# Performance work log

Hardware: AMD Instinct MI355X
Metric: run time of the kernel (lower is better)

Reference implementation:

```python
import jax, jax.numpy as jnp
import numpy as np
import math

B, S, D, H, WIN = 2, 4096, 512, 8, 50
DK = D // H


def setup_inputs() -> dict:
    key = jax.random.key(0)
    ks = jax.random.split(key, 10)
    scale = 0.02
    return {
        "x": jax.random.normal(ks[0], (B, S, D), dtype=jnp.float32),
        "opcode_types": jax.random.randint(ks[1], (B, S), 0, 10, dtype=jnp.int64),
        "Wq": jax.random.normal(ks[2], (D, D), dtype=jnp.float32) * scale,
        "bq": jnp.zeros((D,), dtype=jnp.float32),
        "Wk": jax.random.normal(ks[3], (D, D), dtype=jnp.float32) * scale,
        "bk": jnp.zeros((D,), dtype=jnp.float32),
        "Wv": jax.random.normal(ks[4], (D, D), dtype=jnp.float32) * scale,
        "bv": jnp.zeros((D,), dtype=jnp.float32),
        "Wo": jax.random.normal(ks[5], (D, D), dtype=jnp.float32) * scale,
        "bo": jnp.zeros((D,), dtype=jnp.float32),
    }


def reference(x, opcode_types, Wq, bq, Wk, bk, Wv, bv, Wo, bo):
    b, s, d = x.shape
    # Linear projections (torch Linear: x @ W.T + b), split heads -> [B,H,S,DK]
    q = (x @ Wq.T + bq).reshape(b, s, H, DK).transpose(0, 2, 1, 3)
    k = (x @ Wk.T + bk).reshape(b, s, H, DK).transpose(0, 2, 1, 3)
    v = (x @ Wv.T + bv).reshape(b, s, H, DK).transpose(0, 2, 1, 3)

    pos = jnp.arange(s)
    window = jnp.abs(pos[:, None] - pos[None, :]) <= WIN          # [S,S]
    ctrl_cols = (opcode_types == 0).any(axis=0)                   # [S]
    allow = window | ctrl_cols[None, :]                           # [S,S]

    scores = jnp.einsum("bhqd,bhkd->bhqk", q, k) / math.sqrt(DK)  # [B,H,S,S]
    scores = jnp.where(allow[None, None], scores, jnp.float32(-1e9))
    attn = jax.nn.softmax(scores, axis=-1)
    attn = jnp.nan_to_num(attn, nan=0.0)
    out = jnp.einsum("bhqk,bhkd->bhqd", attn, v)                  # [B,H,S,DK]
    out = out.transpose(0, 2, 1, 3).reshape(b, s, d)
    return out @ Wo.T + bo
```

## Files before the change

kernel.cpp:

```cpp
#include <hip/hip_runtime.h>
#include <hip/hip_bf16.h>
#include <math.h>

#define B_ 2
#define S_ 4096
#define D_ 512
#define H_ 8
#define DK_ 64
#define WIN_ 50
#define NGT 32
#define QSCALE 0.18033688011112042f

typedef __attribute__((ext_vector_type(8))) _Float16 half8;
typedef __attribute__((ext_vector_type(4))) float f32x4;
typedef __attribute__((ext_vector_type(4))) unsigned short us4;
typedef unsigned short ushort_t;

__device__ __forceinline__ unsigned short f2h(float f) {
    _Float16 h = (_Float16)f;
    return __builtin_bit_cast(unsigned short, h);
}
__device__ __forceinline__ unsigned cvt_pk_f16(float lo, float hi) {
    unsigned r;
    asm("v_cvt_pkrtz_f16_f32 %0, %1, %2" : "=v"(r) : "v"(lo), "v"(hi));
    return r;
}
__device__ __forceinline__ float v_exp2(float x) {
    float r;
    asm("v_exp_f32 %0, %1\n\ts_nop 0" : "=v"(r) : "v"(x));
    return r;
}

__global__ __launch_bounds__(256) void prep_all(const float* __restrict__ x,
                                                const float* __restrict__ W0,
                                                const float* __restrict__ W1,
                                                const float* __restrict__ W2,
                                                const float* __restrict__ W3,
                                                const int* __restrict__ opcode,
                                                ushort_t* __restrict__ xh,
                                                ushort_t* __restrict__ whb,
                                                int* __restrict__ glist,
                                                int* __restrict__ gcount) {
    const int bid = blockIdx.x;
    const int t = threadIdx.x;
    if (bid < 4096) {
        int i = bid * 256 + t;
        f32x4 v = ((const f32x4*)x)[i];
        us4 hv;
        for (int e = 0; e < 4; ++e) hv[e] = f2h(v[e]);
        ((us4*)xh)[i] = hv;
    } else if (bid < 5120) {
        int b2 = bid - 4096;
        int wz = b2 >> 8, inner = b2 & 255;
        const float* src = (wz == 0) ? W0 : (wz == 1) ? W1 : (wz == 2) ? W2 : W3;
        int i = inner * 256 + t;
        f32x4 v = ((const f32x4*)src)[i];
        us4 hv;
        for (int e = 0; e < 4; ++e) hv[e] = f2h(v[e]);
        ((us4*)(whb + (size_t)wz * D_ * D_))[i] = hv;
    } else {
        __shared__ int cnts[256];
        unsigned fl = 0; int c = 0;
        for (int k = 0; k < 16; ++k) {
            int col = t * 16 + k;
            int flag = (opcode[col] == 0) | (opcode[S_ + col] == 0);
            fl |= (unsigned)flag << k; c += flag;
        }
        cnts[t] = c;
        __syncthreads();
        for (int off = 1; off < 256; off <<= 1) {
            int v = cnts[t];
            int a = (t >= off) ? cnts[t - off] : 0;
            __syncthreads();
            cnts[t] = v + a;
            __syncthreads();
        }
        int base = cnts[t] - c;
        for (int k = 0; k < 16; ++k)
            if ((fl >> k) & 1) glist[base++] = t * 16 + k;
        int G = cnts[255];
        if (t == 255) gcount[0] = G;
        for (int k = 0; k < 8; ++k) {
            int idx = G + t + k * 256;
            if (idx < S_) glist[idx] = -1;
        }
    }
}

__device__ __forceinline__ void gemm_core1(const ushort_t* __restrict__ A,
                                           const ushort_t* __restrict__ Bw,
                                           ushort_t (&LDS)[2][8192],
                                           int m0, int n0, int t,
                                           f32x4 (&acc)[4][4]) {
    const int lane = t & 63, wave = t >> 6;
    const int lrow = lane & 15, lkg = lane >> 4;
    const int wr = wave >> 1, wc = wave & 1;
    const ushort_t* srcs[2] = {A, Bw};
    const int row0[2] = {m0, n0};

    auto stage = [&](int buf, int k0) {
        #pragma unroll
        for (int it = 0; it < 4; ++it) {
            int c = it * 4 + wave;
            int tile = c >> 3;
            int kg = (c >> 1) & 3;
            int r = ((c & 1) << 6) | lane;
            const ushort_t* g = srcs[tile] + (size_t)(row0[tile] + r) * 512 + k0 + kg * 8;
            __builtin_amdgcn_global_load_lds(
                (const __attribute__((address_space(1))) void*)g,
                (__attribute__((address_space(3))) void*)(&LDS[buf][c * 512]),
                16, 0, 0);
        }
    };

    stage(0, 0);
    __syncthreads();

    const int aoff = lkg * 1024 + (wr * 64 + lrow) * 8;
    const int boff = 4096 + lkg * 1024 + (wc * 64 + lrow) * 8;
    int cur = 0;
    for (int ks = 0; ks < 16; ++ks) {
        if (ks < 15) stage(cur ^ 1, (ks + 1) * 32);
        const ushort_t* Lb = LDS[cur];
        half8 ah[4], bh[4];
        #pragma unroll
        for (int m = 0; m < 4; ++m) ah[m] = *(const half8*)(Lb + aoff + m * 128);
        #pragma unroll
        for (int n = 0; n < 4; ++n) bh[n] = *(const half8*)(Lb + boff + n * 128);
        #pragma unroll
        for (int m = 0; m < 4; ++m)
            #pragma unroll
            for (int n = 0; n < 4; ++n)
                acc[m][n] = __builtin_amdgcn_mfma_f32_16x16x32_f16(ah[m], bh[n], acc[m][n], 0, 0, 0);
        __syncthreads();
        cur ^= 1;
    }
}

__global__ __launch_bounds__(256) void gemm_qkv(const ushort_t* __restrict__ xh,
                                                const ushort_t* __restrict__ whb,
                                                const float* __restrict__ bq,
                                                const float* __restrict__ bk,
                                                const float* __restrict__ bv,
                                                ushort_t* __restrict__ qb,
                                                char* __restrict__ bandimg) {
    __shared__ ushort_t LDS[2][8192];
    const int z = blockIdx.z;
    const int t = threadIdx.x;
    const ushort_t* Wz = whb + (size_t)z * D_ * D_;
    const int lane = t & 63, wave = t >> 6;
    const int lrow = lane & 15, lkg = lane >> 4;
    const int wr = wave >> 1, wc = wave & 1;

    f32x4 acc[4][4];
    for (int m = 0; m < 4; ++m)
        for (int n = 0; n < 4; ++n)
            acc[m][n] = f32x4{0.f, 0.f, 0.f, 0.f};

    if (z == 2) {
        const int m0 = blockIdx.y * 128, n0 = blockIdx.x * 128;
        gemm_core1(xh, Wz, LDS, m0, n0, t, acc);
        for (int m = 0; m < 4; ++m) {
            int s_base = m0 + wr * 64 + m * 16 + lkg * 4;
            int bb = s_base >> 12, s0 = s_base & (S_ - 1);
            int jt = s0 >> 6, jr0 = s0 & 63;
            for (int n = 0; n < 4; ++n) {
                int col = n0 + wc * 64 + n * 16 + lrow;
                float bs = bv[col];
                int hh = col >> 6, dk = col & 63;
                us4 pk;
                for (int r = 0; r < 4; ++r) pk[r] = f2h(acc[m][n][r] + bs);
                char* img = bandimg + (((size_t)(bb * H_ + hh)) * 64 + jt) * 16384 + 8192;
                *(us4*)(img + ((dk * 128 + jr0 * 2) ^ ((dk & 7) << 4))) = pk;
            }
        }
    } else {
        const int m0 = blockIdx.x * 128, n0 = blockIdx.y * 128;
        gemm_core1(Wz, xh, LDS, m0, n0, t, acc);
        const float* bias = (z == 0) ? bq : bk;
        for (int m = 0; m < 4; ++m) {
            int d_base = m0 + wr * 64 + m * 16 + lkg * 4;
            f32x4 b4 = *(const f32x4*)(bias + d_base);
            int hh = d_base >> 6, dkb = d_base & 63;
            for (int n = 0; n < 4; ++n) {
                int s = n0 + wc * 64 + n * 16 + lrow;
                int bb = s >> 12, sl = s & (S_ - 1);
                us4 pk;
                if (z == 0) {
                    for (int r = 0; r < 4; ++r) pk[r] = f2h((acc[m][n][r] + b4[r]) * QSCALE);
                    *(us4*)(qb + (((size_t)(bb * H_ + hh) * S_) + sl) * DK_ + dkb) = pk;
                } else {
                    for (int r = 0; r < 4; ++r) pk[r] = f2h(acc[m][n][r] + b4[r]);
                    int jt = sl >> 6, jr = sl & 63;
                    char* img = bandimg + (((size_t)(bb * H_ + hh)) * 64 + jt) * 16384;
                    *(us4*)(img + ((jr * 128 + dkb * 2) ^ ((jr & 7) << 4))) = pk;
                }
            }
        }
    }
}

__global__ __launch_bounds__(256) void gemm_fin(const ushort_t* __restrict__ Woh,
                                                const ushort_t* __restrict__ aoh,
                                                const float* __restrict__ bias,
                                                float* __restrict__ outp) {
    __shared__ ushort_t LDS[2][6144];
    const int t = threadIdx.x;
    const int lane = t & 63, wave = t >> 6;
    const int lrow = lane & 15, lkg = lane >> 4;
    const int wr = wave >> 1, wc = wave & 1;
    const int m0 = blockIdx.x * 64, n0 = blockIdx.y * 128;

    auto stage = [&](int buf, int k0) {
        #pragma unroll
        for (int it = 0; it < 3; ++it) {
            int c = it * 4 + wave;
            const ushort_t* g;
            if (c < 4) {
                g = Woh + (size_t)(m0 + lane) * 512 + k0 + c * 8;
            } else {
                int s2 = c - 4;
                int kg = s2 >> 1, rh = s2 & 1;
                g = aoh + (size_t)(n0 + rh * 64 + lane) * 512 + k0 + kg * 8;
            }
            __builtin_amdgcn_global_load_lds(
                (const __attribute__((address_space(1))) void*)g,
                (__attribute__((address_space(3))) void*)(&LDS[buf][c * 512]),
                16, 0, 0);
        }
    };

    f32x4 acc[2][4];
    for (int m = 0; m < 2; ++m)
        for (int n = 0; n < 4; ++n)
            acc[m][n] = f32x4{0.f, 0.f, 0.f, 0.f};

    stage(0, 0);
    __syncthreads();

    const int aoff = lkg * 512 + (wr * 32 + lrow) * 8;
    const int boff = 2048 + lkg * 1024 + (wc * 64 + lrow) * 8;
    int cur = 0;
    for (int ks = 0; ks < 16; ++ks) {
        if (ks < 15) stage(cur ^ 1, (ks + 1) * 32);
        const ushort_t* Lb = LDS[cur];
        half8 ah[2], bh[4];
        #pragma unroll
        for (int m = 0; m < 2; ++m) ah[m] = *(const half8*)(Lb + aoff + m * 128);
        #pragma unroll
        for (int n = 0; n < 4; ++n) bh[n] = *(const half8*)(Lb + boff + n * 128);
        #pragma unroll
        for (int m = 0; m < 2; ++m)
            #pragma unroll
            for (int n = 0; n < 4; ++n)
                acc[m][n] = __builtin_amdgcn_mfma_f32_16x16x32_f16(ah[m], bh[n], acc[m][n], 0, 0, 0);
        __syncthreads();
        cur ^= 1;
    }

    for (int m = 0; m < 2; ++m) {
        int d_base = m0 + wr * 32 + m * 16 + lkg * 4;
        f32x4 b4 = *(const f32x4*)(bias + d_base);
        for (int n = 0; n < 4; ++n) {
            int s = n0 + wc * 64 + n * 16 + lrow;
            f32x4 o;
            for (int r = 0; r < 4; ++r) o[r] = acc[m][n][r] + b4[r];
            *(f32x4*)(outp + (size_t)s * D_ + d_base) = o;
        }
    }
}

__global__ __launch_bounds__(256) void prep_glob(const char* __restrict__ bandimg,
                                                 char* __restrict__ globimg,
                                                 const int* __restrict__ glist,
                                                 const int* __restrict__ gcount) {
    int G = gcount[0];
    int gc = blockIdx.x;
    if (gc * 64 >= G) return;
    int h = blockIdx.y, b = blockIdx.z;
    int t = threadIdx.x;
    __shared__ int jl[64];
    if (t < 64) { int gi = gc * 64 + t; jl[t] = (gi < G) ? glist[gi] : -1; }
    __syncthreads();
    const size_t bh = (size_t)(b * H_ + h);
    char* dst = globimg + (bh * NGT + gc) * 16384;
    {
        int c = t >> 2, q = t & 3;
        int jj = jl[c];
        #pragma unroll
        for (int p = 0; p < 2; ++p) {
            int o_dst = c * 128 + q * 32 + p * 16;
            __attribute__((ext_vector_type(8))) short val;
            if (jj >= 0) {
                int jr = jj & 63, jt = jj >> 6;
                const char* src = bandimg + (bh * 64 + jt) * 16384;
                val = *(const __attribute__((ext_vector_type(8))) short*)
                      (src + ((jr * 128 + q * 32 + p * 16) ^ ((jr & 7) << 4)));
            } else {
                for (int e = 0; e < 8; ++e) val[e] = 0;
            }
            *(__attribute__((ext_vector_type(8))) short*)(dst + (o_dst ^ ((c & 7) << 4))) = val;
        }
    }
    {
        int d = t >> 2, qq = t & 3;
        __attribute__((ext_vector_type(8))) short v0, v1;
        #pragma unroll 16
        for (int i = 0; i < 16; ++i) {
            int c = qq * 16 + i;
            int jj = jl[c];
            ushort_t val = 0;
            if (jj >= 0) {
                int jr = jj & 63, jt = jj >> 6;
                const char* src = bandimg + (bh * 64 + jt) * 16384 + 8192;
                val = *(const ushort_t*)(src + ((d * 128 + jr * 2) ^ ((d & 7) << 4)));
            }
            if (i < 8) v0[i] = val; else v1[i - 8] = val;
        }
        int o = d * 128 + qq * 32;
        *(__attribute__((ext_vector_type(8))) short*)(dst + 8192 + (o ^ ((d & 7) << 4))) = v0;
        *(__attribute__((ext_vector_type(8))) short*)(dst + 8192 + ((o + 16) ^ ((d & 7) << 4))) = v1;
    }
}

__global__ __launch_bounds__(512) void attn_mfma6(const ushort_t* __restrict__ Qp,
                                                  const char* __restrict__ bandimg,
                                                  const char* __restrict__ globimg,
                                                  const int* __restrict__ glist,
                                                  const int* __restrict__ gcount,
                                                  ushort_t* __restrict__ AO) {
    __shared__ char buf[2][16384];
    __shared__ ushort_t Ps[8 * 16 * 64];

    const int t = threadIdx.x, lane = t & 63, wave = t >> 6;
    const int q = lane & 15, g = lane >> 4;
    const int bid = blockIdx.x;
    const int bh_lin = bid & 15;
    const int b = bh_lin >> 3, h = bh_lin & 7;
    const int i0 = (bid >> 4) * 128;
    const size_t headoff = ((size_t)(b * H_ + h)) * S_ * DK_;
    const int iq = i0 + wave * 16 + q;
    const int iqm = iq - WIN_;

    half8 qa[2];
    {
        const ushort_t* qrow = Qp + headoff + (size_t)iq * DK_;
        qa[0] = *(const half8*)(qrow + 8 * g);
        qa[1] = *(const half8*)(qrow + 32 + 8 * g);
    }

    f32x4 Oa[4];
    for (int n = 0; n < 4; ++n) Oa[n] = f32x4{0.f, 0.f, 0.f, 0.f};
    float m_st = -1e30f, l_st = 0.f;

    int jlo = i0 - WIN_;
    int jt_lo = (jlo < 0) ? 0 : (jlo >> 6);
    int jhi = i0 + 127 + WIN_; if (jhi > S_ - 1) jhi = S_ - 1;
    int jt_hi = jhi >> 6;
    int nband = jt_hi - jt_lo + 1;
    const int G = gcount[0];
    int nglob = (G + 63) >> 6; if (nglob > NGT) nglob = NGT;
    int nchunk = nband + nglob;

    const size_t bh = (size_t)(b * H_ + h);

    unsigned needmask = 0;
    {
        int wmin = i0 - WIN_, wmax = i0 + 127 + WIN_;
        for (int gc = 0; gc < nglob; ++gc) {
            int lo = glist[gc * 64];
            int hidx = (gc * 64 + 63 < G) ? (gc * 64 + 63) : (G - 1);
            int hi = glist[hidx];
            bool nm = (lo <= wmax && hi >= wmin) || (gc == nglob - 1 && (G & 63));
            needmask |= (unsigned)nm << gc;
        }
    }

    int koff[4][2], poffw[4], poffr[2];
    #pragma unroll
    for (int n = 0; n < 4; ++n) {
        int row = n * 16 + q;
        #pragma unroll
        for (int kt = 0; kt < 2; ++kt)
            koff[n][kt] = (row * 128 + g * 16 + kt * 64) ^ ((row & 7) << 4);
        poffw[n] = (q * 128 + n * 32 + g * 8) ^ ((q & 7) << 4);
    }
    #pragma unroll
    for (int kt = 0; kt < 2; ++kt)
        poffr[kt] = (q * 128 + g * 16 + kt * 64) ^ ((q & 7) << 4);

    const char* band_base = bandimg + (bh * 64 + jt_lo) * 16384;
    const char* glob_base = globimg + (bh * NGT) * 16384;

    auto stage = [&](int ch, int nb) {
        const char* img = (ch < nband) ? (band_base + (size_t)ch * 16384)
                                       : (glob_base + (size_t)(ch - nband) * 16384);
        #pragma unroll
        for (int i = 0; i < 2; ++i) {
            int seg = wave * 2 + i;
            __builtin_amdgcn_global_load_lds(
                (const __attribute__((address_space(1))) void*)(img + seg * 1024 + lane * 16),
                (__attribute__((address_space(3))) void*)(buf[nb] + seg * 1024),
                16, 0, 0);
        }
    };

    stage(0, 0);
    __syncthreads();

    int cur = 0;
    for (int ch = 0; ch < nchunk; ++ch) {
        if (ch + 1 < nchunk) stage(ch + 1, cur ^ 1);
        const bool isband = ch < nband;
        const int cbase = isband ? (jt_lo + ch) * 64 : 0;
        const int gbase = (ch - nband) * 64;
        const char* Kb = buf[cur];
        const char* Vb = buf[cur] + 8192;

        f32x4 sc[4];
        for (int n = 0; n < 4; ++n) sc[n] = f32x4{0.f, 0.f, 0.f, 0.f};
        __builtin_amdgcn_s_setprio(1);
        #pragma unroll
        for (int n = 0; n < 4; ++n)
            #pragma unroll
            for (int kt = 0; kt < 2; ++kt) {
                half8 ka = *(const half8*)(Kb + koff[n][kt]);
                sc[n] = __builtin_amdgcn_mfma_f32_16x16x32_f16(ka, qa[kt], sc[n], 0, 0, 0);
            }
        __builtin_amdgcn_s_setprio(0);

        float pm;
        bool nm = isband || ((needmask >> (ch - nband)) & 1);
        if (nm) {
            pm = -1e30f;
            if (isband) {
                #pragma unroll
                for (int n = 0; n < 4; ++n) {
                    int jb = cbase + n * 16 + 4 * g;
                    #pragma unroll
                    for (int r = 0; r < 4; ++r) {
                        bool inwin = (unsigned)(jb + r - iqm) <= 2 * WIN_;
                        float s = inwin ? sc[n][r] : -1e30f;
                        sc[n][r] = s;
                        pm = fmaxf(pm, s);
                    }
                }
            } else {
                #pragma unroll
                for (int n = 0; n < 4; ++n) {
                    int4 J = *(const int4*)(glist + gbase + n * 16 + g * 4);
                    int js[4] = {J.x, J.y, J.z, J.w};
                    #pragma unroll
                    for (int r = 0; r < 4; ++r) {
                        int jj = js[r];
                        bool inwin = (unsigned)(jj - iqm) <= 2 * WIN_;
                        bool allow = (jj >= 0) && !inwin;
                        float s = allow ? sc[n][r] : -1e30f;
                        sc[n][r] = s;
                        pm = fmaxf(pm, s);
                    }
                }
            }
        } else {
            float a0 = fmaxf(fmaxf(sc[0][0], sc[0][1]), fmaxf(sc[0][2], sc[0][3]));
            float a1 = fmaxf(fmaxf(sc[1][0], sc[1][1]), fmaxf(sc[1][2], sc[1][3]));
            float a2 = fmaxf(fmaxf(sc[2][0], sc[2][1]), fmaxf(sc[2][2], sc[2][3]));
            float a3 = fmaxf(fmaxf(sc[3][0], sc[3][1]), fmaxf(sc[3][2], sc[3][3]));
            pm = fmaxf(fmaxf(a0, a1), fmaxf(a2, a3));
        }
        pm = fmaxf(pm, __shfl_xor(pm, 16, 64));
        pm = fmaxf(pm, __shfl_xor(pm, 32, 64));

        bool skip = __all(pm <= m_st);
        float fac = 1.0f;
        if (!skip) {
            float mn = fmaxf(m_st, pm);
            fac = v_exp2(m_st - mn);
            m_st = mn;
        }
        float rs = 0.f;
        #pragma unroll
        for (int n = 0; n < 4; ++n)
            #pragma unroll
            for (int r = 0; r < 4; ++r) {
                float p = v_exp2(sc[n][r] - m_st);
                sc[n][r] = p;
                rs += p;
            }
        rs += __shfl_xor(rs, 16, 64);
        rs += __shfl_xor(rs, 32, 64);
        l_st = skip ? (l_st + rs) : (l_st * fac + rs);

        ushort_t* Pw = Ps + wave * 1024;
        #pragma unroll
        for (int n = 0; n < 4; ++n) {
            unsigned pk0 = cvt_pk_f16(sc[n][0], sc[n][1]);
            unsigned pk1 = cvt_pk_f16(sc[n][2], sc[n][3]);
            *(unsigned long long*)((char*)Pw + poffw[n]) =
                ((unsigned long long)pk1 << 32) | pk0;
        }

        if (!skip) {
            #pragma unroll
            for (int n = 0; n < 4; ++n)
                #pragma unroll
                for (int r = 0; r < 4; ++r) Oa[n][r] *= fac;
        }

        half8 pa[2];
        #pragma unroll
        for (int kt = 0; kt < 2; ++kt)
            pa[kt] = *(const half8*)((char*)Pw + poffr[kt]);
        __builtin_amdgcn_s_setprio(1);
        #pragma unroll
        for (int n = 0; n < 4; ++n)
            #pragma unroll
            for (int kt = 0; kt < 2; ++kt) {
                half8 va = *(const half8*)(Vb + koff[n][kt]);
                Oa[n] = __builtin_amdgcn_mfma_f32_16x16x32_f16(va, pa[kt], Oa[n], 0, 0, 0);
            }
        __builtin_amdgcn_s_setprio(0);
        __syncthreads();
        cur ^= 1;
    }

    float inv = 1.0f / l_st;
    #pragma unroll
    for (int n = 0; n < 4; ++n) {
        us4 ph;
        #pragma unroll
        for (int r = 0; r < 4; ++r) ph[r] = f2h(Oa[n][r] * inv);
        size_t base = ((size_t)b * S_ + iq) * D_ + h * DK_ + (n * 16 + g * 4);
        *(us4*)(AO + base) = ph;
    }
}

extern "C" void kernel_launch(void* const* d_in, const int* in_sizes, int n_in,
                              void* d_out, int out_size, void* d_ws, size_t ws_size,
                              hipStream_t stream) {
    const float* x      = (const float*)d_in[0];
    const int*   opcode = (const int*)d_in[1];
    const float* Wq = (const float*)d_in[2];
    const float* bq = (const float*)d_in[3];
    const float* Wk = (const float*)d_in[4];
    const float* bk = (const float*)d_in[5];
    const float* Wv = (const float*)d_in[6];
    const float* bv = (const float*)d_in[7];
    const float* Wo = (const float*)d_in[8];
    const float* bo = (const float*)d_in[9];
    float* out = (float*)d_out;

    char* ws = (char*)d_ws;
    const size_t bsd = (size_t)B_ * S_ * D_;
    const size_t hf_bytes = bsd * sizeof(ushort_t);
    const size_t w_bytes  = (size_t)D_ * D_ * sizeof(ushort_t);

    ushort_t* qb = (ushort_t*)(ws);
    ushort_t* xh = (ushort_t*)(ws + hf_bytes);
    ushort_t* ao = xh;
    char* wbase = ws + 2 * hf_bytes;
    ushort_t* whb = (ushort_t*)wbase;
    char* bandimg = wbase + 4 * w_bytes;
    char* globimg = bandimg + (size_t)16 * 64 * 16384;
    int* glist  = (int*)(globimg + (size_t)16 * NGT * 16384);
    int* gcount = glist + S_;

    prep_all<<<5121, 256, 0, stream>>>(x, Wq, Wk, Wv, Wo, opcode,
                                       xh, whb, glist, gcount);

    gemm_qkv<<<dim3(D_ / 128, (B_ * S_) / 128, 3), 256, 0, stream>>>(
        xh, whb, bq, bk, bv, qb, bandimg);

    prep_glob<<<dim3(NGT, H_, B_), 256, 0, stream>>>(bandimg, globimg, glist, gcount);

    attn_mfma6<<<dim3(512), 512, 0, stream>>>(
        qb, bandimg, globimg, glist, gcount, ao);

    gemm_fin<<<dim3(D_ / 64, (B_ * S_) / 128), 256, 0, stream>>>(
        whb + 3 * (size_t)D_ * D_, ao, bo, out);
}
```

Before: 188.6 us.

## Stage GEMM and attention epilogues through LDS for coalesced 16-byte stores

The epilogues of the QKV GEMM, the final GEMM and the attention kernel now write results into shared memory in a swizzled layout, synchronise, and then emit wide 16-byte coalesced global stores. Before, each thread wrote scattered 8-byte or 16-byte fragments. The softmax rescale now fires only when the new max exceeds the running max by more than 8, which cuts the number of rescales. Inline asm for exp2 and pack-convert is replaced with compiler builtins. The cost is extra LDS traffic and barriers, plus a small numerical risk from the lazy rescale threshold.

```diff
diff --git a/kernel.cpp b/kernel.cpp
--- a/kernel.cpp
+++ b/kernel.cpp
@@ -15,20 +15,17 @@
 typedef __attribute__((ext_vector_type(4))) float f32x4;
 typedef __attribute__((ext_vector_type(4))) unsigned short us4;
 typedef unsigned short ushort_t;
+typedef unsigned long long u64;
 
 __device__ __forceinline__ unsigned short f2h(float f) {
     _Float16 h = (_Float16)f;
     return __builtin_bit_cast(unsigned short, h);
 }
 __device__ __forceinline__ unsigned cvt_pk_f16(float lo, float hi) {
-    unsigned r;
-    asm("v_cvt_pkrtz_f16_f32 %0, %1, %2" : "=v"(r) : "v"(lo), "v"(hi));
-    return r;
+    return __builtin_bit_cast(unsigned, __builtin_amdgcn_cvt_pkrtz(lo, hi));
 }
 __device__ __forceinline__ float v_exp2(float x) {
-    float r;
-    asm("v_exp_f32 %0, %1\n\ts_nop 0" : "=v"(r) : "v"(x));
-    return r;
+    return __builtin_amdgcn_exp2f(x);
 }
 
 __global__ __launch_bounds__(256) void prep_all(const float* __restrict__ x,
@@ -157,44 +154,79 @@
         for (int n = 0; n < 4; ++n)
             acc[m][n] = f32x4{0.f, 0.f, 0.f, 0.f};
 
+    char* Lf = (char*)LDS;
+
     if (z == 2) {
         const int m0 = blockIdx.y * 128, n0 = blockIdx.x * 128;
         gemm_core1(xh, Wz, LDS, m0, n0, t, acc);
-        for (int m = 0; m < 4; ++m) {
-            int s_base = m0 + wr * 64 + m * 16 + lkg * 4;
-            int bb = s_base >> 12, s0 = s_base & (S_ - 1);
-            int jt = s0 >> 6, jr0 = s0 & 63;
-            for (int n = 0; n < 4; ++n) {
-                int col = n0 + wc * 64 + n * 16 + lrow;
-                float bs = bv[col];
-                int hh = col >> 6, dk = col & 63;
-                us4 pk;
-                for (int r = 0; r < 4; ++r) pk[r] = f2h(acc[m][n][r] + bs);
-                char* img = bandimg + (((size_t)(bb * H_ + hh)) * 64 + jt) * 16384 + 8192;
-                *(us4*)(img + ((dk * 128 + jr0 * 2) ^ ((dk & 7) << 4))) = pk;
-            }
+        #pragma unroll
+        for (int n = 0; n < 4; ++n) {
+            int dl = wc * 64 + n * 16 + lrow;
+            float bs = bv[n0 + dl];
+            #pragma unroll
+            for (int m = 0; m < 4; ++m) {
+                int sl = wr * 64 + m * 16 + lkg * 4;
+                unsigned pk0 = cvt_pk_f16(acc[m][n][0] + bs, acc[m][n][1] + bs);
+                unsigned pk1 = cvt_pk_f16(acc[m][n][2] + bs, acc[m][n][3] + bs);
+                int off = (dl * 256 + sl * 2) ^ ((dl & 15) << 4);
+                *(u64*)(Lf + off) = ((u64)pk1 << 32) | pk0;
+            }
+        }
+        __syncthreads();
+        int bb = m0 >> 12;
+        int jt0 = (m0 & (S_ - 1)) >> 6;
+        #pragma unroll
+        for (int i = 0; i < 8; ++i) {
+            int L = t + 256 * i;
+            int hd = L >> 10, rem = L & 1023;
+            int jh = rem >> 9, dk = (rem >> 3) & 63, p = rem & 7;
+            int dl = hd * 64 + dk;
+            int off = (dl * 256 + jh * 128 + p * 16) ^ ((dl & 15) << 4);
+            f32x4 v = *(const f32x4*)(Lf + off);
+            int hh = (n0 >> 6) + hd;
+            char* img = bandimg + (((size_t)(bb * H_ + hh)) * 64 + jt0 + jh) * 16384 + 8192;
+            *(f32x4*)(img + ((dk * 128 + p * 16) ^ ((dk & 7) << 4))) = v;
         }
     } else {
         const int m0 = blockIdx.x * 128, n0 = blockIdx.y * 128;
         gemm_core1(Wz, xh, LDS, m0, n0, t, acc);
         const float* bias = (z == 0) ? bq : bk;
+        const float scale = (z == 0) ? QSCALE : 1.0f;
+        #pragma unroll
         for (int m = 0; m < 4; ++m) {
-            int d_base = m0 + wr * 64 + m * 16 + lkg * 4;
-            f32x4 b4 = *(const f32x4*)(bias + d_base);
-            int hh = d_base >> 6, dkb = d_base & 63;
+            int dl = wr * 64 + m * 16 + lkg * 4;
+            f32x4 b4 = *(const f32x4*)(bias + m0 + dl);
+            #pragma unroll
             for (int n = 0; n < 4; ++n) {
-                int s = n0 + wc * 64 + n * 16 + lrow;
-                int bb = s >> 12, sl = s & (S_ - 1);
-                us4 pk;
-                if (z == 0) {
-                    for (int r = 0; r < 4; ++r) pk[r] = f2h((acc[m][n][r] + b4[r]) * QSCALE);
-                    *(us4*)(qb + (((size_t)(bb * H_ + hh) * S_) + sl) * DK_ + dkb) = pk;
-                } else {
-                    for (int r = 0; r < 4; ++r) pk[r] = f2h(acc[m][n][r] + b4[r]);
-                    int jt = sl >> 6, jr = sl & 63;
-                    char* img = bandimg + (((size_t)(bb * H_ + hh)) * 64 + jt) * 16384;
-                    *(us4*)(img + ((jr * 128 + dkb * 2) ^ ((jr & 7) << 4))) = pk;
-                }
+                int sl = wc * 64 + n * 16 + lrow;
+                float v0 = (acc[m][n][0] + b4[0]) * scale;
+                float v1 = (acc[m][n][1] + b4[1]) * scale;
+                float v2 = (acc[m][n][2] + b4[2]) * scale;
+                float v3 = (acc[m][n][3] + b4[3]) * scale;
+                unsigned pk0 = cvt_pk_f16(v0, v1);
+                unsigned pk1 = cvt_pk_f16(v2, v3);
+                int off = (sl * 256 + dl * 2) ^ ((sl & 15) << 4);
+                *(u64*)(Lf + off) = ((u64)pk1 << 32) | pk0;
+            }
+        }
+        __syncthreads();
+        int bb = n0 >> 12;
+        int s0 = n0 & (S_ - 1);
+        #pragma unroll
+        for (int i = 0; i < 8; ++i) {
+            int L = t + 256 * i;
+            int hd = L >> 10, sl = (L >> 3) & 127, p = L & 7;
+            int off = (sl * 256 + hd * 128 + p * 16) ^ ((sl & 15) << 4);
+            f32x4 v = *(const f32x4*)(Lf + off);
+            int hh = (m0 >> 6) + hd;
+            if (z == 0) {
+                char* dst = (char*)qb + (((size_t)(bb * H_ + hh) * S_) + s0 + sl) * DK_ * 2;
+                *(f32x4*)(dst + p * 16) = v;
+            } else {
+                int sg = s0 + sl;
+                int jt = sg >> 6, jr = sg & 63;
+                char* img = bandimg + (((size_t)(bb * H_ + hh)) * 64 + jt) * 16384;
+                *(f32x4*)(img + ((jr * 128 + p * 16) ^ ((jr & 7) << 4))) = v;
             }
         }
     }
@@ -204,7 +236,8 @@
                                                 const ushort_t* __restrict__ aoh,
                                                 const float* __restrict__ bias,
                                                 float* __restrict__ outp) {
-    __shared__ ushort_t LDS[2][6144];
+    __shared__ char LDSF[32768];
+    ushort_t (&LDS)[2][6144] = *reinterpret_cast<ushort_t(*)[2][6144]>(LDSF);
     const int t = threadIdx.x;
     const int lane = t & 63, wave = t >> 6;
     const int lrow = lane & 15, lkg = lane >> 4;
@@ -258,15 +291,26 @@
         cur ^= 1;
     }
 
+    #pragma unroll
     for (int m = 0; m < 2; ++m) {
-        int d_base = m0 + wr * 32 + m * 16 + lkg * 4;
-        f32x4 b4 = *(const f32x4*)(bias + d_base);
+        int dl = wr * 32 + m * 16 + lkg * 4;
+        f32x4 b4 = *(const f32x4*)(bias + m0 + dl);
+        #pragma unroll
         for (int n = 0; n < 4; ++n) {
-            int s = n0 + wc * 64 + n * 16 + lrow;
+            int sl = wc * 64 + n * 16 + lrow;
             f32x4 o;
             for (int r = 0; r < 4; ++r) o[r] = acc[m][n][r] + b4[r];
-            *(f32x4*)(outp + (size_t)s * D_ + d_base) = o;
-        }
+            *(f32x4*)(LDSF + ((sl * 256 + dl * 4) ^ ((sl & 15) << 4))) = o;
+        }
+    }
+    __syncthreads();
+    #pragma unroll
+    for (int i = 0; i < 8; ++i) {
+        int L = t + 256 * i;
+        int sl = L >> 4, p = L & 15;
+        f32x4 v = *(const f32x4*)(LDSF + ((sl * 256 + p * 16) ^ ((sl & 15) << 4)));
+        char* dst = (char*)outp + ((size_t)(n0 + sl) * 512 + m0) * 4;
+        *(f32x4*)(dst + p * 16) = v;
     }
 }
 
@@ -323,7 +367,7 @@
     }
 }
 
-__global__ __launch_bounds__(512) void attn_mfma6(const ushort_t* __restrict__ Qp,
+__global__ __launch_bounds__(512) void attn_mfma8(const ushort_t* __restrict__ Qp,
                                                   const char* __restrict__ bandimg,
                                                   const char* __restrict__ globimg,
                                                   const int* __restrict__ glist,
@@ -471,7 +515,7 @@
         pm = fmaxf(pm, __shfl_xor(pm, 16, 64));
         pm = fmaxf(pm, __shfl_xor(pm, 32, 64));
 
-        bool skip = __all(pm <= m_st);
+        bool skip = __all(pm <= m_st + 8.0f);
         float fac = 1.0f;
         if (!skip) {
             float mn = fmaxf(m_st, pm);
@@ -496,8 +540,7 @@
         for (int n = 0; n < 4; ++n) {
             unsigned pk0 = cvt_pk_f16(sc[n][0], sc[n][1]);
             unsigned pk1 = cvt_pk_f16(sc[n][2], sc[n][3]);
-            *(unsigned long long*)((char*)Pw + poffw[n]) =
-                ((unsigned long long)pk1 << 32) | pk0;
+            *(u64*)((char*)Pw + poffw[n]) = ((u64)pk1 << 32) | pk0;
         }
 
         if (!skip) {
@@ -525,13 +568,27 @@
     }
 
     float inv = 1.0f / l_st;
-    #pragma unroll
-    for (int n = 0; n < 4; ++n) {
-        us4 ph;
-        #pragma unroll
-        for (int r = 0; r < 4; ++r) ph[r] = f2h(Oa[n][r] * inv);
-        size_t base = ((size_t)b * S_ + iq) * D_ + h * DK_ + (n * 16 + g * 4);
-        *(us4*)(AO + base) = ph;
+    {
+        ushort_t* Pw = Ps + wave * 1024;
+        #pragma unroll
+        for (int n = 0; n < 4; ++n) {
+            unsigned pk0 = cvt_pk_f16(Oa[n][0] * inv, Oa[n][1] * inv);
+            unsigned pk1 = cvt_pk_f16(Oa[n][2] * inv, Oa[n][3] * inv);
+            *(u64*)((char*)Pw + poffw[n]) = ((u64)pk1 << 32) | pk0;
+        }
+    }
+    __syncthreads();
+    {
+        const char* Pb = (const char*)Ps;
+        #pragma unroll
+        for (int i = 0; i < 2; ++i) {
+            int L = t + i * 512;
+            int row = L >> 3, p = L & 7;
+            int off = (row * 128 + p * 16) ^ ((row & 7) << 4);
+            f32x4 v = *(const f32x4*)(Pb + off);
+            char* dst = (char*)AO + (((size_t)b * S_ + i0 + row) * D_ + h * DK_) * 2;
+            *(f32x4*)(dst + p * 16) = v;
+        }
     }
 }
 
@@ -573,7 +630,7 @@
 
     prep_glob<<<dim3(NGT, H_, B_), 256, 0, stream>>>(bandimg, globimg, glist, gcount);
 
-    attn_mfma6<<<dim3(512), 512, 0, stream>>>(
+    attn_mfma8<<<dim3(512), 512, 0, stream>>>(
         qb, bandimg, globimg, glist, gcount, ao);
 
     gemm_fin<<<dim3(D_ / 64, (B_ * S_) / 128), 256, 0, stream>>>(
```

New measurement: 184.3 us. 2.3% less time.
